# Performance work log

Measured on AMD Instinct MI355X. Metric: run time of the kernel, lower is better.

Reference implementation:

```python
import jax, jax.numpy as jnp
import numpy as np

N_NODES = 50000
N_EDGES = 600000
N_GRAPHS = 500


def gcn_conv(x, src, dst, W, b, n_nodes):
    # PyG GCNConv: add self-loops, symmetric normalization D^-1/2 (A+I) D^-1/2, then XW + b
    h = x @ W  # [N, F_out]
    loop = jnp.arange(n_nodes)
    s = jnp.concatenate([src, loop])
    d = jnp.concatenate([dst, loop])
    deg = jax.ops.segment_sum(jnp.ones_like(d, dtype=h.dtype), d, num_segments=n_nodes)
    dinv = jnp.where(deg > 0, jax.lax.rsqrt(jnp.maximum(deg, 1.0)), 0.0)
    norm = dinv[s] * dinv[d]  # [E+N]
    msg = h[s] * norm[:, None]  # gather + scale
    out = jax.ops.segment_sum(msg, d, num_segments=n_nodes)  # scatter-add
    return out + b


def setup_inputs() -> dict:
    key = jax.random.key(0)
    ks = jax.random.split(key, 12)
    F_in, H, Hf, D_out = 128, 128, 64, 1
    x = jax.random.normal(ks[0], (N_NODES, F_in), dtype=jnp.float32)
    edge_index = jax.random.randint(ks[1], (2, N_EDGES), 0, N_NODES, dtype=jnp.int64)
    batch = jnp.sort(jax.random.randint(ks[2], (N_NODES,), 0, N_GRAPHS, dtype=jnp.int64))
    def glorot(k, shape):
        lim = np.sqrt(6.0 / (shape[0] + shape[1]))
        return jax.random.uniform(k, shape, jnp.float32, -lim, lim)
    return {
        "x": x, "edge_index": edge_index, "batch": batch,
        "W1": glorot(ks[3], (F_in, H)), "b1": jnp.zeros((H,), jnp.float32),
        "W2": glorot(ks[4], (H, H)), "b2": jnp.zeros((H,), jnp.float32),
        "W3": glorot(ks[5], (H, H)), "b3": jnp.zeros((H,), jnp.float32),
        "Wf1": glorot(ks[6], (H, Hf)), "bf1": jnp.zeros((Hf,), jnp.float32),
        "Wf2": glorot(ks[7], (Hf, D_out)), "bf2": jnp.zeros((D_out,), jnp.float32),
    }


def reference(x, edge_index, batch, W1, b1, W2, b2, W3, b3, Wf1, bf1, Wf2, bf2):
    src, dst = edge_index[0], edge_index[1]
    n = x.shape[0]
    h = jax.nn.relu(gcn_conv(x, src, dst, W1, b1, n))
    h = jax.nn.relu(gcn_conv(h, src, dst, W2, b2, n))
    h = jax.nn.relu(gcn_conv(h, src, dst, W3, b3, n))
    # global_mean_pool: segment mean over graphs
    sums = jax.ops.segment_sum(h, batch, num_segments=N_GRAPHS)
    cnts = jax.ops.segment_sum(jnp.ones((n,), h.dtype), batch, num_segments=N_GRAPHS)
    hg = sums / jnp.maximum(cnts, 1.0)[:, None]  # [G, 128]
    h = jax.nn.relu(hg @ Wf1 + bf1)
    return h @ Wf2 + bf2
```

## Files before the change

### kernel.cpp

```cpp
#include <hip/hip_runtime.h>

#define N_NODES 50000
#define N_EDGES 600000
#define N_GRAPHS 500
#define F 128

typedef short bf16x8 __attribute__((ext_vector_type(8)));
typedef float f32x4 __attribute__((ext_vector_type(4)));
union U4H8 { uint4 u; bf16x8 h; };

__device__ inline unsigned pk_bf16(float a, float b) {
    unsigned ua = __float_as_uint(a), ub = __float_as_uint(b);
    ua = (ua + 0x7fffu + ((ua >> 16) & 1u)) >> 16;
    ub = (ub + 0x7fffu + ((ub >> 16) & 1u)) >> 16;
    return ua | (ub << 16);
}
__device__ inline float bf16_rnd(float x) {
    unsigned u = __float_as_uint(x);
    u = (u + 0x7fffu + ((u >> 16) & 1u)) & 0xffff0000u;
    return __uint_as_float(u);
}
#define BF_LO(u) __uint_as_float((u) << 16)
#define BF_HI(u) __uint_as_float((u) & 0xffff0000u)

#define G_CVT  3125
#define G_HIST 2344
#define G_PREPW 24

__global__ __launch_bounds__(256) void k_prep(const float* __restrict__ x, unsigned short* __restrict__ xb,
                                              const int* __restrict__ dst, int* __restrict__ cnt,
                                              const float* __restrict__ W1, const float* __restrict__ W2,
                                              const float* __restrict__ W3,
                                              uint4* __restrict__ Whi, uint4* __restrict__ Wlo) {
    int b = blockIdx.x, tid = threadIdx.x;
    if (b < G_CVT) {
        int idx = b * 256 + tid;
        if (idx < N_NODES * F / 8) {
            const float4* xr = (const float4*)(x + (size_t)idx * 8);
            float4 a = xr[0], c = xr[1];
            uint4 o;
            o.x = pk_bf16(a.x, a.y); o.y = pk_bf16(a.z, a.w);
            o.z = pk_bf16(c.x, c.y); o.w = pk_bf16(c.z, c.w);
            ((uint4*)xb)[idx] = o;
        }
    } else if (b < G_CVT + G_HIST) {
        int e = (b - G_CVT) * 256 + tid;
        if (e < N_EDGES) atomicAdd(&cnt[dst[e]], 1);
    } else {
        int idx = (b - G_CVT - G_HIST) * 256 + tid;
        int layer = idx >> 11;
        const float* W = (layer == 0) ? W1 : (layer == 1) ? W2 : W3;
        int t = idx & 2047;
        int lane = t & 63, sc = t >> 6;
        int s = sc >> 3, c = sc & 7;
        int q = lane >> 4, m = lane & 15;
        int k0 = 32 * s + 8 * q, n0 = 16 * c + m;
        float w[8], h[8];
        #pragma unroll
        for (int j = 0; j < 8; ++j) {
            w[j] = W[(k0 + j) * F + n0];
            h[j] = bf16_rnd(w[j]);
        }
        uint4 uh, ul;
        uh.x = pk_bf16(h[0], h[1]); uh.y = pk_bf16(h[2], h[3]);
        uh.z = pk_bf16(h[4], h[5]); uh.w = pk_bf16(h[6], h[7]);
        ul.x = pk_bf16(w[0] - h[0], w[1] - h[1]); ul.y = pk_bf16(w[2] - h[2], w[3] - h[3]);
        ul.z = pk_bf16(w[4] - h[4], w[5] - h[5]); ul.w = pk_bf16(w[6] - h[6], w[7] - h[7]);
        Whi[idx] = uh;
        Wlo[idx] = ul;
    }
}

__global__ __launch_bounds__(256) void k_scan1(const int* __restrict__ cnt, int* __restrict__ row_ptr,
                                               int* __restrict__ blksums, float* __restrict__ dinv, int n) {
    __shared__ int s[256];
    int i = blockIdx.x * 256 + threadIdx.x;
    int v = (i < n) ? cnt[i] : 0;
    if (i < n) dinv[i] = rsqrtf((float)(v + 1));
    s[threadIdx.x] = v;
    __syncthreads();
    for (int off = 1; off < 256; off <<= 1) {
        int t = (threadIdx.x >= off) ? s[threadIdx.x - off] : 0;
        __syncthreads();
        s[threadIdx.x] += t;
        __syncthreads();
    }
    if (i < n) row_ptr[i] = s[threadIdx.x] - v;
    if (threadIdx.x == 255) blksums[blockIdx.x] = s[255];
}

__global__ __launch_bounds__(256) void k_scan23(int* __restrict__ row_ptr, const int* __restrict__ blksums,
                                                int n, int ne) {
    __shared__ int s[256];
    int tid = threadIdx.x;
    s[tid] = (tid < (int)blockIdx.x) ? blksums[tid] : 0;
    __syncthreads();
    for (int off = 128; off > 0; off >>= 1) {
        if (tid < off) s[tid] += s[tid + off];
        __syncthreads();
    }
    int base = s[0];
    int i = blockIdx.x * 256 + tid;
    if (i < n) row_ptr[i] += base;
    if (i == 0) row_ptr[n] = ne;
}

__global__ __launch_bounds__(256) void k_fill(const int* __restrict__ src, const int* __restrict__ dst,
                                              const int* __restrict__ row_ptr, int* __restrict__ cnt,
                                              const float* __restrict__ dinv,
                                              int2* __restrict__ esw, int ne) {
    int e = blockIdx.x * 256 + threadIdx.x;
    if (e < ne) {
        int d = dst[e];
        int s = src[e];
        int pos = row_ptr[d] + atomicSub(&cnt[d], 1) - 1;
        esw[pos] = make_int2(s, __float_as_int(dinv[s]));
    }
}

#define TN 32
#define GP 132
#define MAXE_L 1024
__global__ __launch_bounds__(256) void k_fused(const int* __restrict__ row_ptr,
                                               const int2* __restrict__ esw,
                                               const float* __restrict__ dinv,
                                               const unsigned short* __restrict__ Hin,
                                               const uint4* __restrict__ Whi,
                                               const uint4* __restrict__ Wlo,
                                               const float* __restrict__ bias,
                                               unsigned short* __restrict__ Hout, int n) {
    __shared__ float G[TN * GP];
    __shared__ uint2 eL[MAXE_L];
    __shared__ int rp[TN + 1];
    __shared__ float ddl[TN];
    int tid = threadIdx.x;
    int d0 = blockIdx.x * TN;

    int dTN = d0 + TN; if (dTN > n) dTN = n;
    int e0 = row_ptr[d0];
    int e1 = row_ptr[dTN];
    if (tid <= TN) {
        int d = d0 + tid; if (d > n) d = n;
        rp[tid] = row_ptr[d];
    }
    if (tid < TN) {
        int d = d0 + tid;
        ddl[tid] = (d < n) ? dinv[d] : 0.f;
    }
    int nE = e1 - e0; if (nE > MAXE_L) nE = MAXE_L;
    for (int i = tid; i < nE; i += 256) eL[i] = ((const uint2*)esw)[e0 + i];
    __syncthreads();

    int grp = tid >> 4, sub = tid & 15;

    #pragma unroll
    for (int i = 0; i < 2; ++i) {
        int nl = 2 * grp + i;
        int node = d0 + nl;
        float4 accL = make_float4(0.f, 0.f, 0.f, 0.f);
        float4 accH = make_float4(0.f, 0.f, 0.f, 0.f);
        if (node < n) {
            int beg = rp[nl], end = rp[nl + 1];
            float dd = ddl[nl];
            uint4 srow = ((const uint4*)(Hin + (size_t)node * F))[sub];
            float ws = dd * dd;
            accL.x = BF_LO(srow.x) * ws;
            accL.y = BF_HI(srow.x) * ws;
            accL.z = BF_LO(srow.y) * ws;
            accL.w = BF_HI(srow.y) * ws;
            accH.x = BF_LO(srow.z) * ws;
            accH.y = BF_HI(srow.z) * ws;
            accH.z = BF_LO(srow.w) * ws;
            accH.w = BF_HI(srow.w) * ws;
            for (int c = beg; c < end; c += 8) {
                uint2 recs[8];
                #pragma unroll
                for (int j = 0; j < 8; ++j) {
                    int e = c + j;
                    uint2 r = make_uint2((unsigned)node, 0u);
                    if (e < end) {
                        int off = e - e0;
                        r = (off < MAXE_L) ? eL[off] : ((const uint2*)esw)[e];
                    }
                    recs[j] = r;
                }
                uint4 rows[8];
                #pragma unroll
                for (int j = 0; j < 8; ++j)
                    rows[j] = ((const uint4*)(Hin + (size_t)recs[j].x * F))[sub];
                #pragma unroll
                for (int j = 0; j < 8; ++j) {
                    float wj = __uint_as_float(recs[j].y) * dd;
                    accL.x = fmaf(BF_LO(rows[j].x), wj, accL.x);
                    accL.y = fmaf(BF_HI(rows[j].x), wj, accL.y);
                    accL.z = fmaf(BF_LO(rows[j].y), wj, accL.z);
                    accL.w = fmaf(BF_HI(rows[j].y), wj, accL.w);
                    accH.x = fmaf(BF_LO(rows[j].z), wj, accH.x);
                    accH.y = fmaf(BF_HI(rows[j].z), wj, accH.y);
                    accH.z = fmaf(BF_LO(rows[j].w), wj, accH.z);
                    accH.w = fmaf(BF_HI(rows[j].w), wj, accH.w);
                }
            }
        }
        float* gr = &G[nl * GP + 8 * sub];
        ((float4*)gr)[0] = accL;
        ((float4*)gr)[1] = accH;
    }
    __syncthreads();

    int wave = tid >> 6, lane = tid & 63;
    int q = lane >> 4, m = lane & 15;
    int rt = wave & 1;
    int ch = (wave >> 1) * 4;
    int row0 = 16 * rt;
    f32x4 acc[4];
    #pragma unroll
    for (int c = 0; c < 4; ++c) acc[c] = (f32x4){0.f, 0.f, 0.f, 0.f};
    #pragma unroll
    for (int s = 0; s < 4; ++s) {
        const float* gr = &G[(row0 + m) * GP + 32 * s + 8 * q];
        float4 f0 = ((const float4*)gr)[0];
        float4 f1 = ((const float4*)gr)[1];
        float h0 = bf16_rnd(f0.x), h1 = bf16_rnd(f0.y), h2 = bf16_rnd(f0.z), h3 = bf16_rnd(f0.w);
        float h4 = bf16_rnd(f1.x), h5 = bf16_rnd(f1.y), h6 = bf16_rnd(f1.z), h7 = bf16_rnd(f1.w);
        U4H8 ahi, alo;
        ahi.u.x = (__float_as_uint(h0) >> 16) | (__float_as_uint(h1) & 0xffff0000u);
        ahi.u.y = (__float_as_uint(h2) >> 16) | (__float_as_uint(h3) & 0xffff0000u);
        ahi.u.z = (__float_as_uint(h4) >> 16) | (__float_as_uint(h5) & 0xffff0000u);
        ahi.u.w = (__float_as_uint(h6) >> 16) | (__float_as_uint(h7) & 0xffff0000u);
        alo.u.x = pk_bf16(f0.x - h0, f0.y - h1);
        alo.u.y = pk_bf16(f0.z - h2, f0.w - h3);
        alo.u.z = pk_bf16(f1.x - h4, f1.y - h5);
        alo.u.w = pk_bf16(f1.z - h6, f1.w - h7);
        #pragma unroll
        for (int cc = 0; cc < 4; ++cc) {
            int c = ch + cc;
            U4H8 bh, bl;
            bh.u = Whi[(s * 8 + c) * 64 + lane];
            bl.u = Wlo[(s * 8 + c) * 64 + lane];
            acc[cc] = __builtin_amdgcn_mfma_f32_16x16x32_bf16(ahi.h, bh.h, acc[cc], 0, 0, 0);
            acc[cc] = __builtin_amdgcn_mfma_f32_16x16x32_bf16(alo.h, bh.h, acc[cc], 0, 0, 0);
            acc[cc] = __builtin_amdgcn_mfma_f32_16x16x32_bf16(ahi.h, bl.h, acc[cc], 0, 0, 0);
        }
    }
    __syncthreads();

    #pragma unroll
    for (int cc = 0; cc < 4; ++cc) {
        int c = ch + cc;
        float bb = bias[16 * c + m];
        #pragma unroll
        for (int r = 0; r < 4; ++r)
            G[(row0 + 4 * q + r) * GP + 16 * c + m] = fmaxf(acc[cc][r] + bb, 0.f);
    }
    __syncthreads();
    #pragma unroll
    for (int j = 0; j < 2; ++j) {
        int lin = tid + 256 * j;
        int row = lin >> 4, c8 = lin & 15;
        int node = d0 + row;
        if (node < n) {
            const float* gr = &G[row * GP + c8 * 8];
            uint4 o;
            o.x = pk_bf16(gr[0], gr[1]);
            o.y = pk_bf16(gr[2], gr[3]);
            o.z = pk_bf16(gr[4], gr[5]);
            o.w = pk_bf16(gr[6], gr[7]);
            ((uint4*)(Hout + (size_t)node * F))[c8] = o;
        }
    }
}

__global__ __launch_bounds__(256) void k_pool_fc(const unsigned short* __restrict__ Hb,
                                                 const int* __restrict__ batch,
                                                 const float* __restrict__ Wf1,
                                                 const float* __restrict__ bf1,
                                                 const float* __restrict__ Wf2,
                                                 const float* __restrict__ bf2,
                                                 float* __restrict__ out) {
    int g = blockIdx.x;
    int tid = threadIdx.x;
    int lo = 0, hi = N_NODES;
    while (lo < hi) { int mid = (lo + hi) >> 1; if (batch[mid] < g) lo = mid + 1; else hi = mid; }
    int start = lo;
    hi = N_NODES;
    while (lo < hi) { int mid = (lo + hi) >> 1; if (batch[mid] <= g) lo = mid + 1; else hi = mid; }
    int end = lo;

    __shared__ float hs[4][F];
    __shared__ float hg[F];
    int wv = tid >> 6, lane = tid & 63;
    int half = lane >> 5, sub = lane & 31;
    float4 a = make_float4(0.f, 0.f, 0.f, 0.f);
    for (int i = start + wv * 2 + half; i < end; i += 8) {
        uint2 v = ((const uint2*)(Hb + (size_t)i * F))[sub];
        a.x += BF_LO(v.x); a.y += BF_HI(v.x);
        a.z += BF_LO(v.y); a.w += BF_HI(v.y);
    }
    a.x += __shfl_xor(a.x, 32, 64);
    a.y += __shfl_xor(a.y, 32, 64);
    a.z += __shfl_xor(a.z, 32, 64);
    a.w += __shfl_xor(a.w, 32, 64);
    if (half == 0) ((float4*)hs[wv])[sub] = a;
    __syncthreads();
    if (tid < F) {
        float inv = 1.0f / (float)((end - start) > 0 ? (end - start) : 1);
        hg[tid] = (hs[0][tid] + hs[1][tid] + hs[2][tid] + hs[3][tid]) * inv;
    }
    __syncthreads();
    if (tid < 64) {
        float acc = bf1[tid];
        #pragma unroll 4
        for (int f = 0; f < F; ++f) acc = fmaf(hg[f], Wf1[f * 64 + tid], acc);
        float v = fmaxf(acc, 0.f) * Wf2[tid];
        #pragma unroll
        for (int off = 32; off > 0; off >>= 1) v += __shfl_down(v, off, 64);
        if (tid == 0) out[g] = v + bf2[0];
    }
}

extern "C" void kernel_launch(void* const* d_in, const int* in_sizes, int n_in,
                              void* d_out, int out_size, void* d_ws, size_t ws_size,
                              hipStream_t stream) {
    const float* x    = (const float*)d_in[0];
    const int* eidx   = (const int*)d_in[1];
    const int* batch  = (const int*)d_in[2];
    const float* W1   = (const float*)d_in[3];
    const float* b1   = (const float*)d_in[4];
    const float* W2   = (const float*)d_in[5];
    const float* b2   = (const float*)d_in[6];
    const float* W3   = (const float*)d_in[7];
    const float* b3   = (const float*)d_in[8];
    const float* Wf1  = (const float*)d_in[9];
    const float* bf1  = (const float*)d_in[10];
    const float* Wf2  = (const float*)d_in[11];
    const float* bf2  = (const float*)d_in[12];
    float* out = (float*)d_out;

    const int* src = eidx;
    const int* dst = eidx + N_EDGES;

    char* p = (char*)d_ws;
    unsigned short* Xb  = (unsigned short*)p;  p += (size_t)N_NODES * F * 2;
    unsigned short* H1  = (unsigned short*)p;  p += (size_t)N_NODES * F * 2;
    unsigned short* H2  = (unsigned short*)p;  p += (size_t)N_NODES * F * 2;
    unsigned short* H3  = (unsigned short*)p;  p += (size_t)N_NODES * F * 2;
    int2* esw   = (int2*)p;    p += (size_t)N_EDGES * sizeof(int2);
    uint4* Whi  = (uint4*)p;   p += (size_t)3 * 2048 * sizeof(uint4);
    uint4* Wlo  = (uint4*)p;   p += (size_t)3 * 2048 * sizeof(uint4);
    float* dinv = (float*)p;   p += (size_t)N_NODES * sizeof(float);
    int* cnt     = (int*)p;    p += (size_t)N_NODES * sizeof(int);
    int* row_ptr = (int*)p;    p += (size_t)(N_NODES + 1) * sizeof(int);
    int* blksums = (int*)p;    p += 256 * sizeof(int);

    dim3 b256(256);
    int gNodes = (N_NODES + 255) / 256;
    int gEdges = (N_EDGES + 255) / 256;
    int gFused = (N_NODES + TN - 1) / TN;

    hipMemsetAsync(cnt, 0, (size_t)N_NODES * sizeof(int), stream);
    k_prep<<<G_CVT + G_HIST + G_PREPW, b256, 0, stream>>>(x, Xb, dst, cnt, W1, W2, W3, Whi, Wlo);

    k_scan1<<<gNodes, b256, 0, stream>>>(cnt, row_ptr, blksums, dinv, N_NODES);
    k_scan23<<<gNodes, b256, 0, stream>>>(row_ptr, blksums, N_NODES, N_EDGES);
    k_fill<<<gEdges, b256, 0, stream>>>(src, dst, row_ptr, cnt, dinv, esw, N_EDGES);

    k_fused<<<gFused, b256, 0, stream>>>(row_ptr, esw, dinv, Xb, Whi,        Wlo,        b1, H1, N_NODES);
    k_fused<<<gFused, b256, 0, stream>>>(row_ptr, esw, dinv, H1, Whi + 2048, Wlo + 2048, b2, H2, N_NODES);
    k_fused<<<gFused, b256, 0, stream>>>(row_ptr, esw, dinv, H2, Whi + 4096, Wlo + 4096, b3, H3, N_NODES);

    k_pool_fc<<<N_GRAPHS, b256, 0, stream>>>(H3, batch, Wf1, bf1, Wf2, bf2, out);
}
```

Measured before the change: 273.5 us.

## Store aggregated features as bf16 in LDS and drop hi/lo split on activations

```diff
diff --git a/kernel.cpp b/kernel.cpp
--- a/kernel.cpp
+++ b/kernel.cpp
@@ -19,6 +19,10 @@
     unsigned u = __float_as_uint(x);
     u = (u + 0x7fffu + ((u >> 16) & 1u)) & 0xffff0000u;
     return __uint_as_float(u);
+}
+__device__ inline unsigned short bf16_1(float a) {
+    unsigned ua = __float_as_uint(a);
+    return (unsigned short)((ua + 0x7fffu + ((ua >> 16) & 1u)) >> 16);
 }
 #define BF_LO(u) __uint_as_float((u) << 16)
 #define BF_HI(u) __uint_as_float((u) & 0xffff0000u)
@@ -119,17 +123,17 @@
 }
 
 #define TN 32
-#define GP 132
+#define GP2 136
 #define MAXE_L 1024
-__global__ __launch_bounds__(256) void k_fused(const int* __restrict__ row_ptr,
-                                               const int2* __restrict__ esw,
-                                               const float* __restrict__ dinv,
-                                               const unsigned short* __restrict__ Hin,
-                                               const uint4* __restrict__ Whi,
-                                               const uint4* __restrict__ Wlo,
-                                               const float* __restrict__ bias,
-                                               unsigned short* __restrict__ Hout, int n) {
-    __shared__ float G[TN * GP];
+__global__ __launch_bounds__(256, 8) void k_fused(const int* __restrict__ row_ptr,
+                                                  const int2* __restrict__ esw,
+                                                  const float* __restrict__ dinv,
+                                                  const unsigned short* __restrict__ Hin,
+                                                  const uint4* __restrict__ Whi,
+                                                  const uint4* __restrict__ Wlo,
+                                                  const float* __restrict__ bias,
+                                                  unsigned short* __restrict__ Hout, int n) {
+    __shared__ unsigned short Gb[TN * GP2];
     __shared__ uint2 eL[MAXE_L];
     __shared__ int rp[TN + 1];
     __shared__ float ddl[TN];
@@ -173,24 +177,32 @@
             accH.z = BF_LO(srow.w) * ws;
             accH.w = BF_HI(srow.w) * ws;
             for (int c = beg; c < end; c += 8) {
-                uint2 recs[8];
+                int sjs[8];
                 #pragma unroll
                 for (int j = 0; j < 8; ++j) {
                     int e = c + j;
-                    uint2 r = make_uint2((unsigned)node, 0u);
+                    int sj = node;
                     if (e < end) {
                         int off = e - e0;
-                        r = (off < MAXE_L) ? eL[off] : ((const uint2*)esw)[e];
+                        sj = (off < MAXE_L) ? (int)((const unsigned*)eL)[2 * off]
+                                            : ((const uint2*)esw)[e].x;
                     }
-                    recs[j] = r;
+                    sjs[j] = sj;
                 }
                 uint4 rows[8];
                 #pragma unroll
                 for (int j = 0; j < 8; ++j)
-                    rows[j] = ((const uint4*)(Hin + (size_t)recs[j].x * F))[sub];
+                    rows[j] = ((const uint4*)(Hin + (size_t)sjs[j] * F))[sub];
                 #pragma unroll
                 for (int j = 0; j < 8; ++j) {
-                    float wj = __uint_as_float(recs[j].y) * dd;
+                    int e = c + j;
+                    float wj = 0.f;
+                    if (e < end) {
+                        int off = e - e0;
+                        unsigned wb = (off < MAXE_L) ? ((const unsigned*)eL)[2 * off + 1]
+                                                     : (unsigned)((const uint2*)esw)[e].y;
+                        wj = __uint_as_float(wb) * dd;
+                    }
                     accL.x = fmaf(BF_LO(rows[j].x), wj, accL.x);
                     accL.y = fmaf(BF_HI(rows[j].x), wj, accL.y);
                     accL.z = fmaf(BF_LO(rows[j].y), wj, accL.z);
@@ -202,9 +214,12 @@
                 }
             }
         }
-        float* gr = &G[nl * GP + 8 * sub];
-        ((float4*)gr)[0] = accL;
-        ((float4*)gr)[1] = accH;
+        uint4 o;
+        o.x = pk_bf16(accL.x, accL.y);
+        o.y = pk_bf16(accL.z, accL.w);
+        o.z = pk_bf16(accH.x, accH.y);
+        o.w = pk_bf16(accH.z, accH.w);
+        *(uint4*)&Gb[nl * GP2 + 8 * sub] = o;
     }
     __syncthreads();
 
@@ -218,29 +233,16 @@
     for (int c = 0; c < 4; ++c) acc[c] = (f32x4){0.f, 0.f, 0.f, 0.f};
     #pragma unroll
     for (int s = 0; s < 4; ++s) {
-        const float* gr = &G[(row0 + m) * GP + 32 * s + 8 * q];
-        float4 f0 = ((const float4*)gr)[0];
-        float4 f1 = ((const float4*)gr)[1];
-        float h0 = bf16_rnd(f0.x), h1 = bf16_rnd(f0.y), h2 = bf16_rnd(f0.z), h3 = bf16_rnd(f0.w);
-        float h4 = bf16_rnd(f1.x), h5 = bf16_rnd(f1.y), h6 = bf16_rnd(f1.z), h7 = bf16_rnd(f1.w);
-        U4H8 ahi, alo;
-        ahi.u.x = (__float_as_uint(h0) >> 16) | (__float_as_uint(h1) & 0xffff0000u);
-        ahi.u.y = (__float_as_uint(h2) >> 16) | (__float_as_uint(h3) & 0xffff0000u);
-        ahi.u.z = (__float_as_uint(h4) >> 16) | (__float_as_uint(h5) & 0xffff0000u);
-        ahi.u.w = (__float_as_uint(h6) >> 16) | (__float_as_uint(h7) & 0xffff0000u);
-        alo.u.x = pk_bf16(f0.x - h0, f0.y - h1);
-        alo.u.y = pk_bf16(f0.z - h2, f0.w - h3);
-        alo.u.z = pk_bf16(f1.x - h4, f1.y - h5);
-        alo.u.w = pk_bf16(f1.z - h6, f1.w - h7);
+        U4H8 a;
+        a.u = *(const uint4*)&Gb[(row0 + m) * GP2 + 32 * s + 8 * q];
         #pragma unroll
         for (int cc = 0; cc < 4; ++cc) {
             int c = ch + cc;
             U4H8 bh, bl;
             bh.u = Whi[(s * 8 + c) * 64 + lane];
             bl.u = Wlo[(s * 8 + c) * 64 + lane];
-            acc[cc] = __builtin_amdgcn_mfma_f32_16x16x32_bf16(ahi.h, bh.h, acc[cc], 0, 0, 0);
-            acc[cc] = __builtin_amdgcn_mfma_f32_16x16x32_bf16(alo.h, bh.h, acc[cc], 0, 0, 0);
-            acc[cc] = __builtin_amdgcn_mfma_f32_16x16x32_bf16(ahi.h, bl.h, acc[cc], 0, 0, 0);
+            acc[cc] = __builtin_amdgcn_mfma_f32_16x16x32_bf16(a.h, bh.h, acc[cc], 0, 0, 0);
+            acc[cc] = __builtin_amdgcn_mfma_f32_16x16x32_bf16(a.h, bl.h, acc[cc], 0, 0, 0);
         }
     }
     __syncthreads();
@@ -251,7 +253,7 @@
         float bb = bias[16 * c + m];
         #pragma unroll
         for (int r = 0; r < 4; ++r)
-            G[(row0 + 4 * q + r) * GP + 16 * c + m] = fmaxf(acc[cc][r] + bb, 0.f);
+            Gb[(row0 + 4 * q + r) * GP2 + 16 * c + m] = bf16_1(fmaxf(acc[cc][r] + bb, 0.f));
     }
     __syncthreads();
     #pragma unroll
@@ -260,12 +262,7 @@
         int row = lin >> 4, c8 = lin & 15;
         int node = d0 + row;
         if (node < n) {
-            const float* gr = &G[row * GP + c8 * 8];
-            uint4 o;
-            o.x = pk_bf16(gr[0], gr[1]);
-            o.y = pk_bf16(gr[2], gr[3]);
-            o.z = pk_bf16(gr[4], gr[5]);
-            o.w = pk_bf16(gr[6], gr[7]);
+            uint4 o = *(const uint4*)&Gb[row * GP2 + c8 * 8];
             ((uint4*)(Hout + (size_t)node * F))[c8] = o;
         }
     }
```

Result: slower. 324.4 us (+18.6%).
